# Optimization experiments

Measured on AMD Instinct MI355X. Metric: run time of the kernel, lower is better.

## Reference

```python
import math
import jax, jax.numpy as jnp
import numpy as np

LOG2PI = math.log(2.0 * math.pi)


def _log_density_sum(mean, logvar, sample):
    # Gaussian log-density, summed over the trailing feature dim.
    # mean/logvar/sample broadcast against each other.
    inv_sigma = jnp.exp(-logvar)
    tmp = (sample - mean) * inv_sigma
    return jnp.sum(-0.5 * (tmp * tmp + 2.0 * logvar + LOG2PI), axis=-1)


def setup_inputs() -> dict:
    key = jax.random.key(0)
    ks = jax.random.split(key, 6)
    B, T, DF, DZ = 128, 32, 256, 128
    return {
        "f_mean":   jax.random.normal(ks[0], (B, DF), dtype=jnp.float32),
        "f_logvar": jax.random.normal(ks[1], (B, DF), dtype=jnp.float32),
        "f_sample": jax.random.normal(ks[2], (B, DF), dtype=jnp.float32),
        "z_mean":   jax.random.normal(ks[3], (B, T, DZ), dtype=jnp.float32),
        "z_logvar": jax.random.normal(ks[4], (B, T, DZ), dtype=jnp.float32),
        "z_sample": jax.random.normal(ks[5], (B, T, DZ), dtype=jnp.float32),
        "num_train": 50000,
    }


def reference(f_mean, f_logvar, f_sample, z_mean, z_logvar, z_sample, num_train):
    B = f_mean.shape[0]
    log_norm = math.log(B) + math.log(num_train)

    # f pairwise: sample index i vs mean index j -> [B_i, B_j]
    # (original repeats this identically over every step t)
    logq_f_sum = _log_density_sum(
        f_mean[None, :, :], f_logvar[None, :, :], f_sample[:, None, :]
    )  # [B, B]

    # z pairwise per step: transpose to [T, B, D], then [T, B_i, B_j]
    zt_mean = jnp.transpose(z_mean, (1, 0, 2))
    zt_logvar = jnp.transpose(z_logvar, (1, 0, 2))
    zt_sample = jnp.transpose(z_sample, (1, 0, 2))
    logq_z_sum = _log_density_sum(
        zt_mean[:, None, :, :], zt_logvar[:, None, :, :], zt_sample[:, :, None, :]
    )  # [T, B, B]

    # concatenating f and z components along the feature dim then summing
    # equals summing the per-component feature sums
    logq_fz_sum = logq_f_sum[None, :, :] + logq_z_sum  # [T, B, B]

    logq_f = jax.nn.logsumexp(logq_f_sum, axis=1) - log_norm          # [B]
    logq_z = jax.nn.logsumexp(logq_z_sum, axis=2) - log_norm          # [T, B]
    logq_fz = jax.nn.logsumexp(logq_fz_sum, axis=2) - log_norm        # [T, B]

    mi_fz = jnp.mean(jax.nn.relu(logq_fz - logq_f[None, :] - logq_z))
    return mi_fz
```

## Files before the change

kernel.cpp:

```cpp
#include <hip/hip_runtime.h>

#define LOG2PI 1.8378770664093453f



__device__ __forceinline__ float waveReduceSum(float v) {
#pragma unroll
    for (int o = 32; o > 0; o >>= 1) v += __shfl_down(v, o, 64);
    return v;
}

__device__ __forceinline__ float waveReduceMax(float v) {
#pragma unroll
    for (int o = 32; o > 0; o >>= 1) v = fmaxf(v, __shfl_down(v, o, 64));
    return v;
}

__device__ __forceinline__ float blockReduceSum(float v, float* sh) {
    int lane = threadIdx.x & 63, wid = threadIdx.x >> 6, nw = blockDim.x >> 6;
    v = waveReduceSum(v);
    __syncthreads();
    if (lane == 0) sh[wid] = v;
    __syncthreads();
    float r = sh[0];
    for (int w = 1; w < nw; ++w) r += sh[w];
    return r;
}

__device__ __forceinline__ float blockReduceMax(float v, float* sh) {
    int lane = threadIdx.x & 63, wid = threadIdx.x >> 6, nw = blockDim.x >> 6;
    v = waveReduceMax(v);
    __syncthreads();
    if (lane == 0) sh[wid] = v;
    __syncthreads();
    float r = sh[0];
    for (int w = 1; w < nw; ++w) r = fmaxf(r, sh[w]);
    return r;
}

__device__ __forceinline__ float4 halfMax4(float4 v, float4* sh) {
#pragma unroll
    for (int o = 32; o > 0; o >>= 1) {
        v.x = fmaxf(v.x, __shfl_down(v.x, o, 64));
        v.y = fmaxf(v.y, __shfl_down(v.y, o, 64));
        v.z = fmaxf(v.z, __shfl_down(v.z, o, 64));
        v.w = fmaxf(v.w, __shfl_down(v.w, o, 64));
    }
    int wid = threadIdx.x >> 6;
    __syncthreads();
    if ((threadIdx.x & 63) == 0) sh[wid] = v;
    __syncthreads();
    int hb = (threadIdx.x >> 7) << 1;
    float4 a = sh[hb], b = sh[hb + 1];
    return make_float4(fmaxf(a.x, b.x), fmaxf(a.y, b.y),
                       fmaxf(a.z, b.z), fmaxf(a.w, b.w));
}

__device__ __forceinline__ float4 halfSum4(float4 v, float4* sh) {
#pragma unroll
    for (int o = 32; o > 0; o >>= 1) {
        v.x += __shfl_down(v.x, o, 64);
        v.y += __shfl_down(v.y, o, 64);
        v.z += __shfl_down(v.z, o, 64);
        v.w += __shfl_down(v.w, o, 64);
    }
    int wid = threadIdx.x >> 6;
    __syncthreads();
    if ((threadIdx.x & 63) == 0) sh[wid] = v;
    __syncthreads();
    int hb = (threadIdx.x >> 7) << 1;
    float4 a = sh[hb], b = sh[hb + 1];
    return make_float4(a.x + b.x, a.y + b.y, a.z + b.z, a.w + b.w);
}

#define NB_TZ 512
#define NB_TF 32
#define NB_ZS 2048
#define NB_FS 128

__global__ void prep(const float* __restrict__ zm, const float* __restrict__ zlv,
                     const float* __restrict__ fm, const float* __restrict__ flv,
                     float2* __restrict__ zme, float2* __restrict__ fme,
                     float* __restrict__ cz, float* __restrict__ cf,
                     float* __restrict__ out) {
    __shared__ float S[2 * 32 * 33];
    float (*sm)[33] = (float(*)[33])S;
    float (*se)[33] = (float(*)[33])(S + 32 * 33);
    int blk = blockIdx.x;
    int tid = threadIdx.x;

    if (blk < NB_TZ) {
        int t = blk >> 4, bt = (blk >> 2) & 3, dt = blk & 3;
        int tx = tid & 31, ty = tid >> 5;
        int b0 = bt * 32, d0 = dt * 32;
#pragma unroll
        for (int k = 0; k < 4; ++k) {
            int bl = ty + k * 8;
            int idx = (b0 + bl) * 4096 + t * 128 + d0 + tx;
            sm[bl][tx] = zm[idx];
            se[bl][tx] = expf(-2.f * zlv[idx]);
        }
        __syncthreads();
#pragma unroll
        for (int k = 0; k < 4; ++k) {
            int dl = ty + k * 8;
            zme[(t * 128 + d0 + dl) * 128 + b0 + tx] =
                make_float2(sm[tx][dl], se[tx][dl]);
        }
    } else if (blk < NB_TZ + NB_TF) {
        int r = blk - NB_TZ;
        int bt = r >> 3, dt = r & 7;
        int tx = tid & 31, ty = tid >> 5;
        int b0 = bt * 32, d0 = dt * 32;
#pragma unroll
        for (int k = 0; k < 4; ++k) {
            int bl = ty + k * 8;
            int idx = (b0 + bl) * 256 + d0 + tx;
            sm[bl][tx] = fm[idx];
            se[bl][tx] = expf(-2.f * flv[idx]);
        }
        __syncthreads();
#pragma unroll
        for (int k = 0; k < 4; ++k) {
            int dl = ty + k * 8;
            fme[(d0 + dl) * 128 + b0 + tx] = make_float2(sm[tx][dl], se[tx][dl]);
        }
    } else if (blk < NB_TZ + NB_TF + NB_ZS) {
        int r0 = (blk - NB_TZ - NB_TF) * 2;
        int half = tid >> 7, lane = tid & 127;
        int r = r0 + half;
        int b = r >> 5, t = r & 31;
        float v = 2.f * zlv[b * 4096 + t * 128 + lane];
        v = waveReduceSum(v);
        int wid = tid >> 6;
        if ((tid & 63) == 0) S[wid] = v;
        __syncthreads();
        if (tid == 0)   cz[(r0 & 31) * 128 + (r0 >> 5)] = S[0] + S[1];
        if (tid == 128) { int r1 = r0 + 1; cz[(r1 & 31) * 128 + (r1 >> 5)] = S[2] + S[3]; }
    } else if (blk < NB_TZ + NB_TF + NB_ZS + NB_FS) {
        int b = blk - NB_TZ - NB_TF - NB_ZS;
        float v = 2.f * flv[b * 256 + tid];
        v = blockReduceSum(v, S);
        if (tid == 0) cf[b] = v;
    } else {
        if (tid == 0) out[0] = 0.f;
    }
}

__global__ void fker(const float* __restrict__ fs, const float2* __restrict__ fme,
                     const float* __restrict__ cf,
                     float* __restrict__ F, float* __restrict__ lse_f) {
    __shared__ float s_fs[256];
    __shared__ float part[256];
    __shared__ float sh[4];
    int i = blockIdx.x, tid = threadIdx.x;
    int j = tid & 127, dh = tid >> 7;
    s_fs[tid] = fs[i * 256 + tid];
    __syncthreads();
    const float2* fp = fme + dh * 128 * 128;
    const float* ss = s_fs + dh * 128;
    float acc = 0.f;
#pragma unroll 8
    for (int d = 0; d < 128; ++d) {
        float2 me = fp[d * 128 + j];
        float df = ss[d] - me.x;
        acc = fmaf(df * df, me.y, acc);
    }
    part[tid] = acc;
    __syncthreads();
    float Fij = 0.f;
    if (dh == 0) {
        Fij = -0.5f * (acc + part[tid + 128] + cf[j] + 256.f * LOG2PI);
        F[i * 128 + j] = Fij;
    }
    float v = (dh == 0) ? Fij : -INFINITY;
    float m = blockReduceMax(v, sh);
    float e = (dh == 0) ? expf(Fij - m) : 0.f;
    float s = blockReduceSum(e, sh);
    if (tid == 0) lse_f[i] = m + logf(s);
}

__global__ void zker(const float* __restrict__ zs, const float2* __restrict__ zme,
                     const float* __restrict__ cz, const float* __restrict__ F,
                     const float* __restrict__ lse_f, const int* __restrict__ num_train,
                     float* __restrict__ out) {
    __shared__ float s_zs[128 * 8];
    __shared__ float s_acc[2][8][128];
    __shared__ float4 sh4[4];
    int b = blockIdx.x;
    int t = (b & 7) + ((b >> 7) << 3);
    int i0 = ((b >> 3) & 15) * 8;
    int tid = threadIdx.x;
    int j = tid & 127, h = tid >> 7;

#pragma unroll
    for (int kk = 0; kk < 4; ++kk) {
        int k = h * 4 + kk;
        s_zs[j * 8 + k] = zs[(i0 + k) * 4096 + t * 128 + j];
    }
    __syncthreads();

    const float2* zp = zme + t * 16384 + h * 64 * 128;
    float acc[8] = {0.f, 0.f, 0.f, 0.f, 0.f, 0.f, 0.f, 0.f};
#pragma unroll 8
    for (int dd = 0; dd < 64; ++dd) {
        float2 me = zp[dd * 128 + j];
        int d = (h << 6) + dd;
        float4 za = *(const float4*)&s_zs[d * 8];
        float4 zb = *(const float4*)&s_zs[d * 8 + 4];
        float t0;
        t0 = za.x - me.x; acc[0] = fmaf(t0 * t0, me.y, acc[0]);
        t0 = za.y - me.x; acc[1] = fmaf(t0 * t0, me.y, acc[1]);
        t0 = za.z - me.x; acc[2] = fmaf(t0 * t0, me.y, acc[2]);
        t0 = za.w - me.x; acc[3] = fmaf(t0 * t0, me.y, acc[3]);
        t0 = zb.x - me.x; acc[4] = fmaf(t0 * t0, me.y, acc[4]);
        t0 = zb.y - me.x; acc[5] = fmaf(t0 * t0, me.y, acc[5]);
        t0 = zb.z - me.x; acc[6] = fmaf(t0 * t0, me.y, acc[6]);
        t0 = zb.w - me.x; acc[7] = fmaf(t0 * t0, me.y, acc[7]);
    }
#pragma unroll
    for (int k = 0; k < 8; ++k) s_acc[h][k][j] = acc[k];
    __syncthreads();

    int k0 = h * 4;
    float base = -0.5f * (cz[t * 128 + j] + 128.f * LOG2PI);
    float4 rz, fz;
    rz.x = -0.5f * (s_acc[0][k0 + 0][j] + s_acc[1][k0 + 0][j]) + base;
    rz.y = -0.5f * (s_acc[0][k0 + 1][j] + s_acc[1][k0 + 1][j]) + base;
    rz.z = -0.5f * (s_acc[0][k0 + 2][j] + s_acc[1][k0 + 2][j]) + base;
    rz.w = -0.5f * (s_acc[0][k0 + 3][j] + s_acc[1][k0 + 3][j]) + base;
    fz.x = rz.x + F[(i0 + k0 + 0) * 128 + j];
    fz.y = rz.y + F[(i0 + k0 + 1) * 128 + j];
    fz.z = rz.z + F[(i0 + k0 + 2) * 128 + j];
    fz.w = rz.w + F[(i0 + k0 + 3) * 128 + j];

    float4 mz = halfMax4(rz, sh4);
    float4 e = make_float4(expf(rz.x - mz.x), expf(rz.y - mz.y),
                           expf(rz.z - mz.z), expf(rz.w - mz.w));
    float4 sz = halfSum4(e, sh4);
    float4 mf = halfMax4(fz, sh4);
    e = make_float4(expf(fz.x - mf.x), expf(fz.y - mf.y),
                    expf(fz.z - mf.z), expf(fz.w - mf.w));
    float4 sf = halfSum4(e, sh4);

    if (j == 0) {
        float log_norm = logf(128.f * (float)num_train[0]);
        float lz[4] = {mz.x + logf(sz.x), mz.y + logf(sz.y),
                       mz.z + logf(sz.z), mz.w + logf(sz.w)};
        float lfz[4] = {mf.x + logf(sf.x), mf.y + logf(sf.y),
                        mf.z + logf(sf.z), mf.w + logf(sf.w)};
        float s = 0.f;
#pragma unroll
        for (int k = 0; k < 4; ++k) {
            float v = lfz[k] - lse_f[i0 + k0 + k] - lz[k] + log_norm;
            s += (v > 0.f ? v : 0.f);
        }
        atomicAdd(out, s * (1.f / 4096.f));
    }
}

extern "C" void kernel_launch(void* const* d_in, const int* in_sizes, int n_in,
                              void* d_out, int out_size, void* d_ws, size_t ws_size,
                              hipStream_t stream) {
    const float* f_mean    = (const float*)d_in[0];
    const float* f_logvar  = (const float*)d_in[1];
    const float* f_sample  = (const float*)d_in[2];
    const float* z_mean    = (const float*)d_in[3];
    const float* z_logvar  = (const float*)d_in[4];
    const float* z_sample  = (const float*)d_in[5];
    const int*   num_train = (const int*)d_in[6];
    float* out = (float*)d_out;

    float* ws    = (float*)d_ws;
    float2* zme  = (float2*)ws;
    float2* fme  = (float2*)(ws + 1048576);
    float*  cz   = ws + 1048576 + 65536;
    float*  cf   = cz + 4096;
    float*  F    = cf + 128;
    float*  lse_f= F + 16384;

    prep<<<NB_TZ + NB_TF + NB_ZS + NB_FS + 1, 256, 0, stream>>>(
        z_mean, z_logvar, f_mean, f_logvar, zme, fme, cz, cf, out);
    fker<<<128, 256, 0, stream>>>(f_sample, fme, cf, F, lse_f);
    zker<<<512, 256, 0, stream>>>(z_sample, zme, cz, F, lse_f, num_train, out);
}
```

Baseline: 105.2 us.

## Fuse f pairwise kernel into z kernel by recomputing F per block

Removes the separate fker launch and the F/lse_f workspace round-trip. Each zker2 block now recomputes its own 8 rows of the f pairwise density, including their logsumexp, alongside the z accumulation. This trades one kernel launch and a dependency stage for redundant f work: each F row is recomputed by 32 blocks, about twice the per-block arithmetic of the z loop. It also adds extra shared-memory staging and reductions.

```diff
diff --git a/kernel.cpp b/kernel.cpp
--- a/kernel.cpp
+++ b/kernel.cpp
@@ -7,12 +7,6 @@
 __device__ __forceinline__ float waveReduceSum(float v) {
 #pragma unroll
     for (int o = 32; o > 0; o >>= 1) v += __shfl_down(v, o, 64);
-    return v;
-}
-
-__device__ __forceinline__ float waveReduceMax(float v) {
-#pragma unroll
-    for (int o = 32; o > 0; o >>= 1) v = fmaxf(v, __shfl_down(v, o, 64));
     return v;
 }
 
@@ -24,17 +18,6 @@
     __syncthreads();
     float r = sh[0];
     for (int w = 1; w < nw; ++w) r += sh[w];
-    return r;
-}
-
-__device__ __forceinline__ float blockReduceMax(float v, float* sh) {
-    int lane = threadIdx.x & 63, wid = threadIdx.x >> 6, nw = blockDim.x >> 6;
-    v = waveReduceMax(v);
-    __syncthreads();
-    if (lane == 0) sh[wid] = v;
-    __syncthreads();
-    float r = sh[0];
-    for (int w = 1; w < nw; ++w) r = fmaxf(r, sh[w]);
     return r;
 }
 
@@ -147,44 +130,13 @@
     }
 }
 
-__global__ void fker(const float* __restrict__ fs, const float2* __restrict__ fme,
-                     const float* __restrict__ cf,
-                     float* __restrict__ F, float* __restrict__ lse_f) {
-    __shared__ float s_fs[256];
-    __shared__ float part[256];
-    __shared__ float sh[4];
-    int i = blockIdx.x, tid = threadIdx.x;
-    int j = tid & 127, dh = tid >> 7;
-    s_fs[tid] = fs[i * 256 + tid];
-    __syncthreads();
-    const float2* fp = fme + dh * 128 * 128;
-    const float* ss = s_fs + dh * 128;
-    float acc = 0.f;
-#pragma unroll 8
-    for (int d = 0; d < 128; ++d) {
-        float2 me = fp[d * 128 + j];
-        float df = ss[d] - me.x;
-        acc = fmaf(df * df, me.y, acc);
-    }
-    part[tid] = acc;
-    __syncthreads();
-    float Fij = 0.f;
-    if (dh == 0) {
-        Fij = -0.5f * (acc + part[tid + 128] + cf[j] + 256.f * LOG2PI);
-        F[i * 128 + j] = Fij;
-    }
-    float v = (dh == 0) ? Fij : -INFINITY;
-    float m = blockReduceMax(v, sh);
-    float e = (dh == 0) ? expf(Fij - m) : 0.f;
-    float s = blockReduceSum(e, sh);
-    if (tid == 0) lse_f[i] = m + logf(s);
-}
-
-__global__ void zker(const float* __restrict__ zs, const float2* __restrict__ zme,
-                     const float* __restrict__ cz, const float* __restrict__ F,
-                     const float* __restrict__ lse_f, const int* __restrict__ num_train,
-                     float* __restrict__ out) {
+__global__ __launch_bounds__(256) void zker2(
+        const float* __restrict__ zs, const float* __restrict__ fs,
+        const float2* __restrict__ zme, const float2* __restrict__ fme,
+        const float* __restrict__ cz, const float* __restrict__ cf,
+        const int* __restrict__ num_train, float* __restrict__ out) {
     __shared__ float s_zs[128 * 8];
+    __shared__ float s_fs[256 * 8];
     __shared__ float s_acc[2][8][128];
     __shared__ float4 sh4[4];
     int b = blockIdx.x;
@@ -198,46 +150,80 @@
         int k = h * 4 + kk;
         s_zs[j * 8 + k] = zs[(i0 + k) * 4096 + t * 128 + j];
     }
+#pragma unroll
+    for (int k = 0; k < 8; ++k)
+        s_fs[tid * 8 + k] = fs[(i0 + k) * 256 + tid];
     __syncthreads();
 
     const float2* zp = zme + t * 16384 + h * 64 * 128;
-    float acc[8] = {0.f, 0.f, 0.f, 0.f, 0.f, 0.f, 0.f, 0.f};
+    float accz[8] = {0.f, 0.f, 0.f, 0.f, 0.f, 0.f, 0.f, 0.f};
 #pragma unroll 8
     for (int dd = 0; dd < 64; ++dd) {
         float2 me = zp[dd * 128 + j];
         int d = (h << 6) + dd;
         float4 za = *(const float4*)&s_zs[d * 8];
         float4 zb = *(const float4*)&s_zs[d * 8 + 4];
-        float t0;
-        t0 = za.x - me.x; acc[0] = fmaf(t0 * t0, me.y, acc[0]);
-        t0 = za.y - me.x; acc[1] = fmaf(t0 * t0, me.y, acc[1]);
-        t0 = za.z - me.x; acc[2] = fmaf(t0 * t0, me.y, acc[2]);
-        t0 = za.w - me.x; acc[3] = fmaf(t0 * t0, me.y, acc[3]);
-        t0 = zb.x - me.x; acc[4] = fmaf(t0 * t0, me.y, acc[4]);
-        t0 = zb.y - me.x; acc[5] = fmaf(t0 * t0, me.y, acc[5]);
-        t0 = zb.z - me.x; acc[6] = fmaf(t0 * t0, me.y, acc[6]);
-        t0 = zb.w - me.x; acc[7] = fmaf(t0 * t0, me.y, acc[7]);
-    }
-#pragma unroll
-    for (int k = 0; k < 8; ++k) s_acc[h][k][j] = acc[k];
-    __syncthreads();
-
+        float u;
+        u = za.x - me.x; accz[0] = fmaf(u * u, me.y, accz[0]);
+        u = za.y - me.x; accz[1] = fmaf(u * u, me.y, accz[1]);
+        u = za.z - me.x; accz[2] = fmaf(u * u, me.y, accz[2]);
+        u = za.w - me.x; accz[3] = fmaf(u * u, me.y, accz[3]);
+        u = zb.x - me.x; accz[4] = fmaf(u * u, me.y, accz[4]);
+        u = zb.y - me.x; accz[5] = fmaf(u * u, me.y, accz[5]);
+        u = zb.z - me.x; accz[6] = fmaf(u * u, me.y, accz[6]);
+        u = zb.w - me.x; accz[7] = fmaf(u * u, me.y, accz[7]);
+    }
+
+    const float2* fp = fme + h * 128 * 128;
+    float accf[8] = {0.f, 0.f, 0.f, 0.f, 0.f, 0.f, 0.f, 0.f};
+#pragma unroll 4
+    for (int dd = 0; dd < 128; ++dd) {
+        float2 me = fp[dd * 128 + j];
+        int d = (h << 7) + dd;
+        float4 fa = *(const float4*)&s_fs[d * 8];
+        float4 fb = *(const float4*)&s_fs[d * 8 + 4];
+        float u;
+        u = fa.x - me.x; accf[0] = fmaf(u * u, me.y, accf[0]);
+        u = fa.y - me.x; accf[1] = fmaf(u * u, me.y, accf[1]);
+        u = fa.z - me.x; accf[2] = fmaf(u * u, me.y, accf[2]);
+        u = fa.w - me.x; accf[3] = fmaf(u * u, me.y, accf[3]);
+        u = fb.x - me.x; accf[4] = fmaf(u * u, me.y, accf[4]);
+        u = fb.y - me.x; accf[5] = fmaf(u * u, me.y, accf[5]);
+        u = fb.z - me.x; accf[6] = fmaf(u * u, me.y, accf[6]);
+        u = fb.w - me.x; accf[7] = fmaf(u * u, me.y, accf[7]);
+    }
+
+#pragma unroll
+    for (int k = 0; k < 8; ++k) s_acc[h][k][j] = accz[k];
+    __syncthreads();
     int k0 = h * 4;
     float base = -0.5f * (cz[t * 128 + j] + 128.f * LOG2PI);
-    float4 rz, fz;
+    float4 rz;
     rz.x = -0.5f * (s_acc[0][k0 + 0][j] + s_acc[1][k0 + 0][j]) + base;
     rz.y = -0.5f * (s_acc[0][k0 + 1][j] + s_acc[1][k0 + 1][j]) + base;
     rz.z = -0.5f * (s_acc[0][k0 + 2][j] + s_acc[1][k0 + 2][j]) + base;
     rz.w = -0.5f * (s_acc[0][k0 + 3][j] + s_acc[1][k0 + 3][j]) + base;
-    fz.x = rz.x + F[(i0 + k0 + 0) * 128 + j];
-    fz.y = rz.y + F[(i0 + k0 + 1) * 128 + j];
-    fz.z = rz.z + F[(i0 + k0 + 2) * 128 + j];
-    fz.w = rz.w + F[(i0 + k0 + 3) * 128 + j];
+    __syncthreads();
+
+#pragma unroll
+    for (int k = 0; k < 8; ++k) s_acc[h][k][j] = accf[k];
+    __syncthreads();
+    float cfb = -0.5f * (cf[j] + 256.f * LOG2PI);
+    float4 F4;
+    F4.x = -0.5f * (s_acc[0][k0 + 0][j] + s_acc[1][k0 + 0][j]) + cfb;
+    F4.y = -0.5f * (s_acc[0][k0 + 1][j] + s_acc[1][k0 + 1][j]) + cfb;
+    F4.z = -0.5f * (s_acc[0][k0 + 2][j] + s_acc[1][k0 + 2][j]) + cfb;
+    F4.w = -0.5f * (s_acc[0][k0 + 3][j] + s_acc[1][k0 + 3][j]) + cfb;
+    float4 fz = make_float4(rz.x + F4.x, rz.y + F4.y, rz.z + F4.z, rz.w + F4.w);
 
     float4 mz = halfMax4(rz, sh4);
     float4 e = make_float4(expf(rz.x - mz.x), expf(rz.y - mz.y),
                            expf(rz.z - mz.z), expf(rz.w - mz.w));
     float4 sz = halfSum4(e, sh4);
+    float4 mF = halfMax4(F4, sh4);
+    e = make_float4(expf(F4.x - mF.x), expf(F4.y - mF.y),
+                    expf(F4.z - mF.z), expf(F4.w - mF.w));
+    float4 sF = halfSum4(e, sh4);
     float4 mf = halfMax4(fz, sh4);
     e = make_float4(expf(fz.x - mf.x), expf(fz.y - mf.y),
                     expf(fz.z - mf.z), expf(fz.w - mf.w));
@@ -245,14 +231,16 @@
 
     if (j == 0) {
         float log_norm = logf(128.f * (float)num_train[0]);
-        float lz[4] = {mz.x + logf(sz.x), mz.y + logf(sz.y),
-                       mz.z + logf(sz.z), mz.w + logf(sz.w)};
+        float lz[4]  = {mz.x + logf(sz.x), mz.y + logf(sz.y),
+                        mz.z + logf(sz.z), mz.w + logf(sz.w)};
+        float lF[4]  = {mF.x + logf(sF.x), mF.y + logf(sF.y),
+                        mF.z + logf(sF.z), mF.w + logf(sF.w)};
         float lfz[4] = {mf.x + logf(sf.x), mf.y + logf(sf.y),
                         mf.z + logf(sf.z), mf.w + logf(sf.w)};
         float s = 0.f;
 #pragma unroll
         for (int k = 0; k < 4; ++k) {
-            float v = lfz[k] - lse_f[i0 + k0 + k] - lz[k] + log_norm;
+            float v = lfz[k] - lF[k] - lz[k] + log_norm;
             s += (v > 0.f ? v : 0.f);
         }
         atomicAdd(out, s * (1.f / 4096.f));
@@ -276,11 +264,9 @@
     float2* fme  = (float2*)(ws + 1048576);
     float*  cz   = ws + 1048576 + 65536;
     float*  cf   = cz + 4096;
-    float*  F    = cf + 128;
-    float*  lse_f= F + 16384;
 
     prep<<<NB_TZ + NB_TF + NB_ZS + NB_FS + 1, 256, 0, stream>>>(
         z_mean, z_logvar, f_mean, f_logvar, zme, fme, cz, cf, out);
-    fker<<<128, 256, 0, stream>>>(f_sample, fme, cf, F, lse_f);
-    zker<<<512, 256, 0, stream>>>(z_sample, zme, cz, F, lse_f, num_train, out);
-}
+    zker2<<<512, 256, 0, stream>>>(z_sample, f_sample, zme, fme, cz, cf,
+                                   num_train, out);
+}
```

After: 107.4 us. 2.1% more time.
